# Optimization experiments

Measured on AMD Instinct MI355X. Metric: run time of the kernel, lower is better.

The kernel has to match this reference:

```python
import jax, jax.numpy as jnp
import numpy as np

NUM_EMBEDDINGS = 512
EMBEDDING_DIM = 256
COMMITMENT_COST = 0.5
DECAY = 0.99
EPSILON = 1e-05


def setup_inputs() -> dict:
    key = jax.random.key(0)
    k1, k2, k3 = jax.random.split(key, 3)
    z_e = jax.random.normal(k1, (16, 256, 16, 16, 16), dtype=jnp.float32)
    codebook = jax.random.normal(k2, (NUM_EMBEDDINGS, EMBEDDING_DIM), dtype=jnp.float32)
    ema_cluster_size = jnp.ones((NUM_EMBEDDINGS,), dtype=jnp.float32)
    ema_embed_sum = jax.random.normal(k3, (NUM_EMBEDDINGS, EMBEDDING_DIM), dtype=jnp.float32)
    return {"z_e": z_e, "codebook": codebook,
            "ema_cluster_size": ema_cluster_size, "ema_embed_sum": ema_embed_sum}


def reference(z_e, codebook, ema_cluster_size, ema_embed_sum):
    B, C, D, H, W = z_e.shape
    K = codebook.shape[0]
    # [B, D, H, W, C] -> [N, C]
    z_perm = jnp.transpose(z_e, (0, 2, 3, 4, 1))
    flat = z_perm.reshape(-1, C)

    # squared-distance argmin: ||z||^2 + ||e||^2 - 2 z.e  (N x K)
    z_sq = jnp.sum(flat * flat, axis=1, keepdims=True)          # [N, 1]
    e_sq = jnp.sum(codebook * codebook, axis=1)[None, :]        # [1, K]
    dot = flat @ codebook.T                                      # [N, K]
    distances = z_sq + e_sq - 2.0 * dot
    encoding_indices = jnp.argmin(distances, axis=1)             # [N]

    z_q_flat = codebook[encoding_indices]                        # gather lookup

    # EMA statistics (training-mode buffer updates; dead-code reset omitted
    # since it is driven by a host-side randperm).
    batch_cluster_size = jax.ops.segment_sum(
        jnp.ones_like(encoding_indices, dtype=flat.dtype), encoding_indices,
        num_segments=K)
    batch_embed_sum = jax.ops.segment_sum(flat, encoding_indices, num_segments=K)
    new_cluster_size = DECAY * ema_cluster_size + (1.0 - DECAY) * batch_cluster_size
    new_embed_sum = DECAY * ema_embed_sum + (1.0 - DECAY) * batch_embed_sum
    n = jnp.sum(new_cluster_size)
    smoothed = (new_cluster_size + EPSILON) / (n + K * EPSILON) * n
    new_codebook = new_embed_sum / smoothed[:, None]

    z_q_perm = z_q_flat.reshape(z_perm.shape)
    commitment_loss = jnp.mean((z_perm - jax.lax.stop_gradient(z_q_perm)) ** 2)
    vq_loss = COMMITMENT_COST * commitment_loss

    # straight-through estimator
    z_q_st = z_perm + jax.lax.stop_gradient(z_q_perm - z_perm)
    z_q = jnp.transpose(z_q_st, (0, 4, 1, 2, 3))
    indices_out = encoding_indices.reshape(B, D, H, W)
    return (z_q, vq_loss, indices_out, new_codebook, new_cluster_size, new_embed_sum)
```

## Files before the change

kernel.cpp:

```cpp
#include <hip/hip_runtime.h>
#include <cfloat>

#define K_NUM 512
#define C_DIM 256

#define WS_CNT    0
#define WS_ESQ    512
#define WS_SMOOTH 1024
#define WS_LOSS   1536
#define WS_CBT    2048
#define WS_ACC    133120

#define OFF_LOSS 16777216
#define OFF_IDX  16777217
#define OFF_CB   16842753
#define OFF_CS   16973825
#define OFF_ES   16974337

__device__ __forceinline__ void gl_lds16(const float* g, float* l) {
  __builtin_amdgcn_global_load_lds(
      (const __attribute__((address_space(1))) unsigned int*)g,
      (__attribute__((address_space(3))) unsigned int*)l, 16, 0, 0);
}

__global__ __launch_bounds__(256) void k0a_prep(const float* __restrict__ cb,
                                                float* __restrict__ ws) {
  int k = blockIdx.x, c = threadIdx.x;
  float v = cb[k * C_DIM + c];
  float s = v * v;
  #pragma unroll
  for (int o = 32; o > 0; o >>= 1) s += __shfl_down(s, o, 64);
  __shared__ float ls[4];
  if ((c & 63) == 0) ls[c >> 6] = s;
  __syncthreads();
  if (c == 0) {
    ws[WS_ESQ + k] = ls[0] + ls[1] + ls[2] + ls[3];
    ws[WS_CNT + k] = 0.f;
    if (k == 0) ws[WS_LOSS] = 0.f;
  }
}

__global__ __launch_bounds__(256) void k0b_transpose(const float* __restrict__ cb,
                                                     float* __restrict__ cbT) {
  __shared__ float t[64 * 69];
  int tid = threadIdx.x;
  int k0 = (blockIdx.x >> 2) * 64;
  int c0 = (blockIdx.x & 3) * 64;
  {
    int kk = tid >> 4, cq = tid & 15;
    #pragma unroll
    for (int r = 0; r < 4; ++r) {
      int row = kk + 16 * r;
      float4 v = *(const float4*)&cb[(size_t)(k0 + row) * C_DIM + c0 + 4 * cq];
      float* p = &t[row * 69 + 4 * cq];
      p[0] = v.x; p[1] = v.y; p[2] = v.z; p[3] = v.w;
    }
  }
  __syncthreads();
  {
    int kq = tid & 15, cc = tid >> 4;
    #pragma unroll
    for (int r = 0; r < 4; ++r) {
      int c = cc + 16 * r;
      float4 v;
      v.x = t[(4 * kq + 0) * 69 + c];
      v.y = t[(4 * kq + 1) * 69 + c];
      v.z = t[(4 * kq + 2) * 69 + c];
      v.w = t[(4 * kq + 3) * 69 + c];
      *(float4*)&cbT[(size_t)(c0 + c) * K_NUM + k0 + 4 * kq] = v;
    }
  }
}

#define STAGE_CT(buf, skc, sc8) do {                                          \
    int c0_ = (sc8) << 4;                                                     \
    _Pragma("unroll")                                                         \
    for (int r_ = 0; r_ < 2; ++r_) {                                          \
      int i4_ = tid + (r_ << 8);                                              \
      gl_lds16(cbT + ((size_t)(c0_ + (i4_ >> 5)) << 9) + ((skc) << 7)         \
                   + ((i4_ & 31) << 2),                                       \
               &ct[((buf) << 11) + (i4_ << 2)]);                              \
    }                                                                         \
  } while (0)

__global__ __launch_bounds__(256) void k1_gemm(const float* __restrict__ z,
                                               const float* __restrict__ cb,
                                               float* __restrict__ out,
                                               float* __restrict__ ws) {
  __shared__ __align__(16) float zt[256 * 128];
  __shared__ __align__(16) float ct[2 * 16 * 128];
  __shared__ __align__(16) int   s_fidx[128];
  __shared__ float s_fmv[128];
  __shared__ float s_ls[4];

  const float* cbT = ws + WS_CBT;
  const float* esq = ws + WS_ESQ;

  int tid = threadIdx.x;
  int nb = blockIdx.x << 7;
  int b = nb >> 12;
  int d = (nb >> 8) & 15;
  int off = nb & 255;
  size_t base = (size_t)b * 1048576 + (size_t)d * 256 + off;
  const float* zbase = z + base;

  int wn = tid >> 4;
  int wk = tid & 15;

  #pragma unroll 8
  for (int r = 0; r < 32; ++r) {
    int idx4 = tid + (r << 8);
    gl_lds16(zbase + ((size_t)(idx4 >> 5) << 12) + ((idx4 & 31) << 2),
             &zt[idx4 << 2]);
  }
  STAGE_CT(0, 0, 0);
  __syncthreads();

  float minv[8]; int mini[8];
  #pragma unroll
  for (int i = 0; i < 8; ++i) { minv[i] = FLT_MAX; mini[i] = 0; }

  int cur = 0;
  for (int kc = 0; kc < 4; ++kc) {
    float acc[8][8];
    #pragma unroll
    for (int i = 0; i < 8; ++i)
      #pragma unroll
      for (int j = 0; j < 8; ++j) acc[i][j] = 0.f;

    for (int c8 = 0; c8 < 16; ++c8) {
      int nc8 = c8 + 1, nkc = kc + (nc8 >> 4); nc8 &= 15;
      if (nkc < 4) STAGE_CT(cur ^ 1, nkc, nc8);
      const float* ctb = &ct[cur << 11];
      #pragma unroll 4
      for (int cc = 0; cc < 16; ++cc) {
        int c = (c8 << 4) + cc;
        float4 za = *(const float4*)&zt[c * 128 + 4 * wn];
        float4 zb = *(const float4*)&zt[c * 128 + 64 + 4 * wn];
        float4 ca = *(const float4*)&ctb[cc * 128 + 4 * wk];
        float4 cb4 = *(const float4*)&ctb[cc * 128 + 64 + 4 * wk];
        float zr[8] = {za.x, za.y, za.z, za.w, zb.x, zb.y, zb.z, zb.w};
        float cr[8] = {ca.x, ca.y, ca.z, ca.w, cb4.x, cb4.y, cb4.z, cb4.w};
        #pragma unroll
        for (int i = 0; i < 8; ++i)
          #pragma unroll
          for (int j = 0; j < 8; ++j) acc[i][j] += zr[i] * cr[j];
      }
      __syncthreads();
      cur ^= 1;
    }
    #pragma unroll
    for (int j = 0; j < 8; ++j) {
      int kg = kc * 128 + (j >> 2) * 64 + 4 * wk + (j & 3);
      float er = esq[kg];
      #pragma unroll
      for (int i = 0; i < 8; ++i) {
        float val = er - 2.f * acc[i][j];
        if (val < minv[i] || (val == minv[i] && kg < mini[i])) { minv[i] = val; mini[i] = kg; }
      }
    }
  }
  #pragma unroll
  for (int i = 0; i < 8; ++i) {
    float v = minv[i]; int ii = mini[i];
    #pragma unroll
    for (int o = 8; o > 0; o >>= 1) {
      float ov = __shfl_xor(v, o, 16);
      int   oi = __shfl_xor(ii, o, 16);
      if (ov < v || (ov == v && oi < ii)) { v = ov; ii = oi; }
    }
    if (wk == i) {
      int n = (i >> 2) * 64 + 4 * wn + (i & 3);
      s_fidx[n] = ii; s_fmv[n] = v;
      out[OFF_IDX + nb + n] = (float)ii;
    }
  }
  __syncthreads();
  int j4 = (tid & 31) * 4;
  int ch = tid >> 5;
  int4 idxs = *(const int4*)&s_fidx[j4];
  const float* r0 = cb + (size_t)idxs.x * C_DIM;
  const float* r1 = cb + (size_t)idxs.y * C_DIM;
  const float* r2 = cb + (size_t)idxs.z * C_DIM;
  const float* r3 = cb + (size_t)idxs.w * C_DIM;
  float zsq = 0.f;
  #pragma unroll 4
  for (int i = 0; i < 32; ++i) {
    int c = ch + 8 * i;
    float4 zv = *(const float4*)&zt[c * 128 + j4];
    float4 q = make_float4(r0[c], r1[c], r2[c], r3[c]);
    *(float4*)(out + base + (size_t)c * 4096 + j4) = q;
    zsq += zv.x * zv.x + zv.y * zv.y + zv.z * zv.z + zv.w * zv.w;
  }
  if (tid < 128) zsq += s_fmv[tid];
  #pragma unroll
  for (int o = 32; o > 0; o >>= 1) zsq += __shfl_down(zsq, o, 64);
  if ((tid & 63) == 0) s_ls[tid >> 6] = zsq;
  __syncthreads();
  if (tid == 0) unsafeAtomicAdd(&ws[WS_LOSS], s_ls[0] + s_ls[1] + s_ls[2] + s_ls[3]);
}

__global__ __launch_bounds__(256) void k1b_scatter(const float* __restrict__ z,
                                                   const float* __restrict__ out,
                                                   float* __restrict__ ws, int n_per) {
  __shared__ float tab[K_NUM * 65];
  float* counts = ws + WS_CNT;
  float* myTab = ws + WS_ACC + (size_t)blockIdx.x * (K_NUM * C_DIM);

  int tid = threadIdx.x;
  int nb = blockIdx.x * n_per;

  for (int pass = 0; pass < 4; ++pass) {
    int cq = pass * 64;
    for (int i = tid; i < K_NUM * 65; i += 256) tab[i] = 0.f;
    __syncthreads();

    for (int nn = tid * 2; nn < n_per; nn += 512) {
      int n0 = nb + nn;
      int i0 = (int)out[OFF_IDX + n0];
      int i1 = (int)out[OFF_IDX + n0 + 1];
      if (pass == 0) {
        unsafeAtomicAdd(&counts[i0], 1.f);
        unsafeAtomicAdd(&counts[i1], 1.f);
      }
      int a0 = i0 * 65, a1 = i1 * 65;
      size_t basez = (size_t)(n0 >> 12) * 1048576 + (size_t)(n0 & 4095);
      const float* zp = z + basez + (size_t)cq * 4096;
      #pragma unroll 8
      for (int cl = 0; cl < 64; ++cl) {
        float2 zv = *(const float2*)(zp + (size_t)cl * 4096);
        __hip_atomic_fetch_add(&tab[a0 + cl], zv.x, __ATOMIC_RELAXED,
                               __HIP_MEMORY_SCOPE_WORKGROUP);
        __hip_atomic_fetch_add(&tab[a1 + cl], zv.y, __ATOMIC_RELAXED,
                               __HIP_MEMORY_SCOPE_WORKGROUP);
      }
    }
    __syncthreads();
    int cl = tid & 63, kr = tid >> 6;
    for (int k0 = 0; k0 < K_NUM; k0 += 4) {
      int k = k0 + kr;
      myTab[k * C_DIM + cq + cl] = tab[k * 65 + cl];
    }
    __syncthreads();
  }
}

__global__ __launch_bounds__(512) void k2_cluster(const float* __restrict__ ema_cs,
                                                  float* __restrict__ out,
                                                  float* __restrict__ ws) {
  int k = threadIdx.x;
  float ncs = 0.99f * ema_cs[k] + 0.01f * ws[WS_CNT + k];
  out[OFF_CS + k] = ncs;
  float s = ncs;
  #pragma unroll
  for (int o = 32; o > 0; o >>= 1) s += __shfl_down(s, o, 64);
  __shared__ float ls[8];
  __shared__ float ntot;
  if ((k & 63) == 0) ls[k >> 6] = s;
  __syncthreads();
  if (k == 0) {
    float n = 0.f;
    #pragma unroll
    for (int i = 0; i < 8; ++i) n += ls[i];
    ntot = n;
    out[OFF_LOSS] = 0.5f * ws[WS_LOSS] / 16777216.f;
  }
  __syncthreads();
  float n = ntot;
  ws[WS_SMOOTH + k] = (ncs + 1e-5f) / (n + 0.00512f) * n;
}

__global__ __launch_bounds__(256) void k3_embed(const float* __restrict__ ema_es,
                                                float* __restrict__ out,
                                                const float* __restrict__ ws, int nblk) {
  int k = blockIdx.x, c = threadIdx.x;
  int i = k * C_DIM + c;
  float bs = 0.f;
  for (int t = 0; t < nblk; ++t) bs += ws[WS_ACC + (size_t)t * (K_NUM * C_DIM) + i];
  float es = 0.99f * ema_es[i] + 0.01f * bs;
  out[OFF_ES + i] = es;
  out[OFF_CB + i] = es / ws[WS_SMOOTH + k];
}

extern "C" void kernel_launch(void* const* d_in, const int* in_sizes, int n_in,
                              void* d_out, int out_size, void* d_ws, size_t ws_size,
                              hipStream_t stream) {
  const float* z      = (const float*)d_in[0];
  const float* cb     = (const float*)d_in[1];
  const float* ema_cs = (const float*)d_in[2];
  const float* ema_es = (const float*)d_in[3];
  float* out = (float*)d_out;
  float* ws  = (float*)d_ws;

  size_t avail = ws_size / 4;
  int nblk = 128;
  while (nblk > 8 && (size_t)WS_ACC + (size_t)nblk * (K_NUM * C_DIM) > avail) nblk >>= 1;
  int n_per = 65536 / nblk;

  k0a_prep<<<512, 256, 0, stream>>>(cb, ws);
  k0b_transpose<<<32, 256, 0, stream>>>(cb, ws + WS_CBT);
  k1_gemm<<<512, 256, 0, stream>>>(z, cb, out, ws);
  k1b_scatter<<<nblk, 256, 0, stream>>>(z, out, ws, n_per);
  k2_cluster<<<1, 512, 0, stream>>>(ema_cs, out, ws);
  k3_embed<<<512, 256, 0, stream>>>(ema_es, out, ws, nblk);
}
```

Baseline: 699.0 us.

## Retile distance GEMM over all codes per thread and widen scatter blocks

The distance GEMM now uses 512-thread blocks, and each thread accumulates a 16x8 tile covering all 512 codes in a single pass. The argmin epilogue runs once at the end with a full-wave shuffle reduction instead of once per 128-code chunk. The scatter kernel moves to 1024-thread blocks with half as many blocks, and counts go into shared memory before a single global atomic per code. This aims to improve reuse and cut per-chunk overhead and global atomics. The trade-offs are higher register pressure (128 accumulators), fewer scatter blocks in flight, and LDS atomic contention.

```diff
diff --git a/kernel.cpp b/kernel.cpp
--- a/kernel.cpp
+++ b/kernel.cpp
@@ -72,26 +72,22 @@
   }
 }
 
-#define STAGE_CT(buf, skc, sc8) do {                                          \
-    int c0_ = (sc8) << 4;                                                     \
-    _Pragma("unroll")                                                         \
-    for (int r_ = 0; r_ < 2; ++r_) {                                          \
-      int i4_ = tid + (r_ << 8);                                              \
-      gl_lds16(cbT + ((size_t)(c0_ + (i4_ >> 5)) << 9) + ((skc) << 7)         \
-                   + ((i4_ & 31) << 2),                                       \
-               &ct[((buf) << 11) + (i4_ << 2)]);                              \
-    }                                                                         \
+#define STAGE_CT(buf, s) do {                                                 \
+    int cc_ = tid >> 7;                                                       \
+    int k4_ = (tid & 127) << 2;                                               \
+    gl_lds16(cbT + (((size_t)((s) << 2) + cc_) << 9) + k4_,                   \
+             &ct[((buf) << 11) + (tid << 2)]);                                \
   } while (0)
 
-__global__ __launch_bounds__(256) void k1_gemm(const float* __restrict__ z,
-                                               const float* __restrict__ cb,
-                                               float* __restrict__ out,
-                                               float* __restrict__ ws) {
+__global__ __launch_bounds__(512, 2) void k1_gemm(const float* __restrict__ z,
+                                                  const float* __restrict__ cb,
+                                                  float* __restrict__ out,
+                                                  float* __restrict__ ws) {
   __shared__ __align__(16) float zt[256 * 128];
-  __shared__ __align__(16) float ct[2 * 16 * 128];
+  __shared__ __align__(16) float ct[2 * 4 * 512];
   __shared__ __align__(16) int   s_fidx[128];
   __shared__ float s_fmv[128];
-  __shared__ float s_ls[4];
+  __shared__ float s_ls[8];
 
   const float* cbT = ws + WS_CBT;
   const float* esq = ws + WS_ESQ;
@@ -104,73 +100,74 @@
   size_t base = (size_t)b * 1048576 + (size_t)d * 256 + off;
   const float* zbase = z + base;
 
-  int wn = tid >> 4;
-  int wk = tid & 15;
-
-  #pragma unroll 8
-  for (int r = 0; r < 32; ++r) {
-    int idx4 = tid + (r << 8);
+  int wn = tid >> 6;
+  int wk = tid & 63;
+
+  #pragma unroll 4
+  for (int r = 0; r < 16; ++r) {
+    int idx4 = tid + (r << 9);
     gl_lds16(zbase + ((size_t)(idx4 >> 5) << 12) + ((idx4 & 31) << 2),
              &zt[idx4 << 2]);
   }
-  STAGE_CT(0, 0, 0);
-  __syncthreads();
-
-  float minv[8]; int mini[8];
-  #pragma unroll
-  for (int i = 0; i < 8; ++i) { minv[i] = FLT_MAX; mini[i] = 0; }
+  STAGE_CT(0, 0);
+  __syncthreads();
+
+  float acc[16][8];
+  #pragma unroll
+  for (int i = 0; i < 16; ++i)
+    #pragma unroll
+    for (int j = 0; j < 8; ++j) acc[i][j] = 0.f;
 
   int cur = 0;
-  for (int kc = 0; kc < 4; ++kc) {
-    float acc[8][8];
-    #pragma unroll
-    for (int i = 0; i < 8; ++i)
+  for (int s = 0; s < 64; ++s) {
+    if (s < 63) STAGE_CT(cur ^ 1, s + 1);
+    const float* ctb = &ct[cur << 11];
+    #pragma unroll
+    for (int cc = 0; cc < 4; ++cc) {
+      int c = (s << 2) + cc;
+      const float* zr0 = &zt[c * 128 + 16 * wn];
+      float4 z0 = *(const float4*)(zr0);
+      float4 z1 = *(const float4*)(zr0 + 4);
+      float4 z2 = *(const float4*)(zr0 + 8);
+      float4 z3 = *(const float4*)(zr0 + 12);
+      float4 ca = *(const float4*)&ctb[cc * 512 + 4 * wk];
+      float4 cb4 = *(const float4*)&ctb[cc * 512 + 256 + 4 * wk];
+      float zr[16] = {z0.x, z0.y, z0.z, z0.w, z1.x, z1.y, z1.z, z1.w,
+                      z2.x, z2.y, z2.z, z2.w, z3.x, z3.y, z3.z, z3.w};
+      float cr[8]  = {ca.x, ca.y, ca.z, ca.w, cb4.x, cb4.y, cb4.z, cb4.w};
       #pragma unroll
-      for (int j = 0; j < 8; ++j) acc[i][j] = 0.f;
-
-    for (int c8 = 0; c8 < 16; ++c8) {
-      int nc8 = c8 + 1, nkc = kc + (nc8 >> 4); nc8 &= 15;
-      if (nkc < 4) STAGE_CT(cur ^ 1, nkc, nc8);
-      const float* ctb = &ct[cur << 11];
-      #pragma unroll 4
-      for (int cc = 0; cc < 16; ++cc) {
-        int c = (c8 << 4) + cc;
-        float4 za = *(const float4*)&zt[c * 128 + 4 * wn];
-        float4 zb = *(const float4*)&zt[c * 128 + 64 + 4 * wn];
-        float4 ca = *(const float4*)&ctb[cc * 128 + 4 * wk];
-        float4 cb4 = *(const float4*)&ctb[cc * 128 + 64 + 4 * wk];
-        float zr[8] = {za.x, za.y, za.z, za.w, zb.x, zb.y, zb.z, zb.w};
-        float cr[8] = {ca.x, ca.y, ca.z, ca.w, cb4.x, cb4.y, cb4.z, cb4.w};
+      for (int i = 0; i < 16; ++i)
         #pragma unroll
-        for (int i = 0; i < 8; ++i)
-          #pragma unroll
-          for (int j = 0; j < 8; ++j) acc[i][j] += zr[i] * cr[j];
-      }
-      __syncthreads();
-      cur ^= 1;
-    }
-    #pragma unroll
-    for (int j = 0; j < 8; ++j) {
-      int kg = kc * 128 + (j >> 2) * 64 + 4 * wk + (j & 3);
-      float er = esq[kg];
-      #pragma unroll
-      for (int i = 0; i < 8; ++i) {
-        float val = er - 2.f * acc[i][j];
-        if (val < minv[i] || (val == minv[i] && kg < mini[i])) { minv[i] = val; mini[i] = kg; }
-      }
-    }
-  }
-  #pragma unroll
-  for (int i = 0; i < 8; ++i) {
+        for (int j = 0; j < 8; ++j) acc[i][j] += zr[i] * cr[j];
+    }
+    __syncthreads();
+    cur ^= 1;
+  }
+
+  float minv[16]; int mini[16];
+  #pragma unroll
+  for (int i = 0; i < 16; ++i) { minv[i] = FLT_MAX; mini[i] = 0; }
+  #pragma unroll
+  for (int j = 0; j < 8; ++j) {
+    int kg = ((j >> 2) << 8) + 4 * wk + (j & 3);
+    float er = esq[kg];
+    #pragma unroll
+    for (int i = 0; i < 16; ++i) {
+      float val = er - 2.f * acc[i][j];
+      if (val < minv[i] || (val == minv[i] && kg < mini[i])) { minv[i] = val; mini[i] = kg; }
+    }
+  }
+  #pragma unroll
+  for (int i = 0; i < 16; ++i) {
     float v = minv[i]; int ii = mini[i];
     #pragma unroll
-    for (int o = 8; o > 0; o >>= 1) {
-      float ov = __shfl_xor(v, o, 16);
-      int   oi = __shfl_xor(ii, o, 16);
+    for (int o = 32; o > 0; o >>= 1) {
+      float ov = __shfl_xor(v, o, 64);
+      int   oi = __shfl_xor(ii, o, 64);
       if (ov < v || (ov == v && oi < ii)) { v = ov; ii = oi; }
     }
     if (wk == i) {
-      int n = (i >> 2) * 64 + 4 * wn + (i & 3);
+      int n = 16 * wn + i;
       s_fidx[n] = ii; s_fmv[n] = v;
       out[OFF_IDX + nb + n] = (float)ii;
     }
@@ -185,8 +182,8 @@
   const float* r3 = cb + (size_t)idxs.w * C_DIM;
   float zsq = 0.f;
   #pragma unroll 4
-  for (int i = 0; i < 32; ++i) {
-    int c = ch + 8 * i;
+  for (int i = 0; i < 16; ++i) {
+    int c = ch + 16 * i;
     float4 zv = *(const float4*)&zt[c * 128 + j4];
     float4 q = make_float4(r0[c], r1[c], r2[c], r3[c]);
     *(float4*)(out + base + (size_t)c * 4096 + j4) = q;
@@ -197,52 +194,55 @@
   for (int o = 32; o > 0; o >>= 1) zsq += __shfl_down(zsq, o, 64);
   if ((tid & 63) == 0) s_ls[tid >> 6] = zsq;
   __syncthreads();
-  if (tid == 0) unsafeAtomicAdd(&ws[WS_LOSS], s_ls[0] + s_ls[1] + s_ls[2] + s_ls[3]);
-}
-
-__global__ __launch_bounds__(256) void k1b_scatter(const float* __restrict__ z,
-                                                   const float* __restrict__ out,
-                                                   float* __restrict__ ws, int n_per) {
+  if (tid == 0) {
+    float t = 0.f;
+    #pragma unroll
+    for (int i = 0; i < 8; ++i) t += s_ls[i];
+    unsafeAtomicAdd(&ws[WS_LOSS], t);
+  }
+}
+
+__global__ __launch_bounds__(1024) void k1b_scatter(const float* __restrict__ z,
+                                                    const float* __restrict__ out,
+                                                    float* __restrict__ ws, int n_per) {
   __shared__ float tab[K_NUM * 65];
+  __shared__ float cnt[K_NUM];
   float* counts = ws + WS_CNT;
   float* myTab = ws + WS_ACC + (size_t)blockIdx.x * (K_NUM * C_DIM);
 
   int tid = threadIdx.x;
   int nb = blockIdx.x * n_per;
+  if (tid < K_NUM) cnt[tid] = 0.f;
 
   for (int pass = 0; pass < 4; ++pass) {
-    int cq = pass * 64;
-    for (int i = tid; i < K_NUM * 65; i += 256) tab[i] = 0.f;
+    int cq = pass << 6;
+    for (int i = tid; i < K_NUM * 65; i += 1024) tab[i] = 0.f;
     __syncthreads();
 
-    for (int nn = tid * 2; nn < n_per; nn += 512) {
+    for (int nn = tid; nn < n_per; nn += 1024) {
       int n0 = nb + nn;
-      int i0 = (int)out[OFF_IDX + n0];
-      int i1 = (int)out[OFF_IDX + n0 + 1];
-      if (pass == 0) {
-        unsafeAtomicAdd(&counts[i0], 1.f);
-        unsafeAtomicAdd(&counts[i1], 1.f);
-      }
-      int a0 = i0 * 65, a1 = i1 * 65;
+      int idx = (int)out[OFF_IDX + n0];
+      if (pass == 0)
+        __hip_atomic_fetch_add(&cnt[idx], 1.f, __ATOMIC_RELAXED,
+                               __HIP_MEMORY_SCOPE_WORKGROUP);
+      int a0 = idx * 65;
       size_t basez = (size_t)(n0 >> 12) * 1048576 + (size_t)(n0 & 4095);
       const float* zp = z + basez + (size_t)cq * 4096;
       #pragma unroll 8
       for (int cl = 0; cl < 64; ++cl) {
-        float2 zv = *(const float2*)(zp + (size_t)cl * 4096);
-        __hip_atomic_fetch_add(&tab[a0 + cl], zv.x, __ATOMIC_RELAXED,
-                               __HIP_MEMORY_SCOPE_WORKGROUP);
-        __hip_atomic_fetch_add(&tab[a1 + cl], zv.y, __ATOMIC_RELAXED,
-                               __HIP_MEMORY_SCOPE_WORKGROUP);
+        __hip_atomic_fetch_add(&tab[a0 + cl], zp[(size_t)cl * 4096],
+                               __ATOMIC_RELAXED, __HIP_MEMORY_SCOPE_WORKGROUP);
       }
     }
     __syncthreads();
     int cl = tid & 63, kr = tid >> 6;
-    for (int k0 = 0; k0 < K_NUM; k0 += 4) {
+    for (int k0 = 0; k0 < K_NUM; k0 += 16) {
       int k = k0 + kr;
       myTab[k * C_DIM + cq + cl] = tab[k * 65 + cl];
     }
     __syncthreads();
   }
+  if (tid < K_NUM) unsafeAtomicAdd(&counts[tid], cnt[tid]);
 }
 
 __global__ __launch_bounds__(512) void k2_cluster(const float* __restrict__ ema_cs,
@@ -293,14 +293,14 @@
   float* ws  = (float*)d_ws;
 
   size_t avail = ws_size / 4;
-  int nblk = 128;
+  int nblk = 64;
   while (nblk > 8 && (size_t)WS_ACC + (size_t)nblk * (K_NUM * C_DIM) > avail) nblk >>= 1;
   int n_per = 65536 / nblk;
 
   k0a_prep<<<512, 256, 0, stream>>>(cb, ws);
   k0b_transpose<<<32, 256, 0, stream>>>(cb, ws + WS_CBT);
-  k1_gemm<<<512, 256, 0, stream>>>(z, cb, out, ws);
-  k1b_scatter<<<nblk, 256, 0, stream>>>(z, out, ws, n_per);
+  k1_gemm<<<512, 512, 0, stream>>>(z, cb, out, ws);
+  k1b_scatter<<<nblk, 1024, 0, stream>>>(z, out, ws, n_per);
   k2_cluster<<<1, 512, 0, stream>>>(ema_cs, out, ws);
   k3_embed<<<512, 256, 0, stream>>>(ema_es, out, ws, nblk);
 }
```

Result: slower. 752.4 us (+7.7%).
